# Optimization experiments

Hardware: AMD Instinct MI355X
Metric: run time of the kernel (lower is better)

Reference implementation:

```python
import jax, jax.numpy as jnp
import numpy as np

EPS = 1e-7
BLOCK_SIZE = 128
LN_EPS = 1e-6

def _project(x):
    norm = jnp.maximum(jnp.linalg.norm(x, axis=-1, keepdims=True), EPS)
    max_norm = 1.0 - EPS
    return jnp.where(norm >= 1.0, x / norm * max_norm, x)

def _mobius_add(x, y, c):
    x2 = jnp.sum(x * x, -1, keepdims=True)
    y2 = jnp.sum(y * y, -1, keepdims=True)
    xy = jnp.sum(x * y, -1, keepdims=True)
    num = (1 + 2 * c * xy + c * y2) * x + (1 - c * x2) * y
    den = 1 + 2 * c * xy + c * c * x2 * y2
    return _project(num / jnp.maximum(den, EPS))

def _logmap0(y, c):
    sqrt_c = jnp.maximum(jnp.sqrt(c), EPS)
    y_norm = jnp.linalg.norm(y, axis=-1, keepdims=True)
    safe = jnp.maximum(y_norm, EPS)
    mag = jnp.arctanh(jnp.minimum(y_norm, 1.0 - EPS)) / sqrt_c
    return jnp.where(y_norm < EPS, jnp.zeros_like(y), mag * (y / safe))

def _expmap0(v, c):
    sqrt_c = jnp.maximum(jnp.sqrt(c), EPS)
    v_norm = jnp.linalg.norm(v, axis=-1, keepdims=True)
    safe = jnp.maximum(v_norm, EPS)
    mag = jnp.tanh(sqrt_c * safe) / sqrt_c
    return _project(jnp.where(v_norm < EPS, jnp.zeros_like(v), mag * (v / safe)))

def _dist(x, y, c):
    sqrt_c = jnp.maximum(jnp.sqrt(c), EPS)
    add_norm = jnp.linalg.norm(_mobius_add(-x, y, c), axis=-1)
    sc = jnp.squeeze(sqrt_c, -1)
    arg = jnp.minimum(sc * add_norm, 1.0 - EPS)
    return 2.0 * jnp.arctanh(arg) / sc

def _layernorm(t, scale, bias):
    mu = jnp.mean(t, -1, keepdims=True)
    var = jnp.mean((t - mu) ** 2, -1, keepdims=True)
    return (t - mu) * jax.lax.rsqrt(var + LN_EPS) * scale + bias

def _rope(x, fc):
    # x: [Be, H, bs, hd]; fc: [bs, hd//2] complex
    x_r, x_i = jnp.split(x, 2, -1)
    xc = jax.lax.complex(x_r, x_i)
    rot = xc * fc.reshape(1, 1, fc.shape[0], fc.shape[1])
    return jnp.concatenate([rot.real, rot.imag], -1)

def setup_inputs() -> dict:
    key = jax.random.key(0)
    ks = jax.random.split(key, 8)
    B, N, D, H = 1, 1024, 1024, 16
    w = lambda k, s: jax.random.normal(k, s, jnp.float32) * 0.02
    x = jax.random.normal(ks[0], (B, N, D), jnp.float32) * 0.02  # points inside the ball
    c_global = jax.random.uniform(ks[1], (B, 1), jnp.float32, minval=0.1, maxval=1.0)
    return dict(
        x=x, c_global=c_global,
        qkv_w=w(ks[2], (D, 3 * D)), qkv_b=jnp.zeros((3 * D,), jnp.float32),
        out_w=w(ks[3], (D, D)), out_b=jnp.zeros((D,), jnp.float32),
        ffn_w1=w(ks[4], (D, 4 * D)), ffn_b1=jnp.zeros((4 * D,), jnp.float32),
        ffn_w2=w(ks[5], (4 * D, D)), ffn_b2=jnp.zeros((D,), jnp.float32),
        ln1_scale=jnp.ones((D,), jnp.float32), ln1_bias=jnp.zeros((D,), jnp.float32),
        ln2_scale=jnp.ones((D,), jnp.float32), ln2_bias=jnp.zeros((D,), jnp.float32),
        c_logits=jnp.zeros((H,), jnp.float32),
        geo_scale=jnp.ones((1, H, 1, 1), jnp.float32),
        start_pos=0,
    )

def reference(x, c_global, qkv_w, qkv_b, out_w, out_b, ffn_w1, ffn_b1, ffn_w2, ffn_b2,
              ln1_scale, ln1_bias, ln2_scale, ln2_bias, c_logits, geo_scale, start_pos):
    B, N, D = x.shape
    H = c_logits.shape[0]
    hd = D // H
    bs = BLOCK_SIZE
    nb = N // bs
    Be = B * nb
    xb = x.reshape(Be, bs, D)
    c_b = jnp.repeat(c_global, nb, axis=0).reshape(Be, 1, 1)
    x_res1 = xb
    # tangent-space norm 1 + attention input
    x_norm = _expmap0(_layernorm(_logmap0(xb, c_b), ln1_scale, ln1_bias), c_b)
    x_tan = _logmap0(x_norm, c_b)
    qkv = (x_tan @ qkv_w + qkv_b).reshape(Be, bs, 3, H, hd).transpose(2, 0, 3, 1, 4)
    q, k, v = qkv[0], qkv[1], qkv[2]  # [Be, H, bs, hd]
    # block-local RoPE (module recomputes freqs_cis for h_dim/block_size internally)
    freqs = 1.0 / (10000.0 ** (jnp.arange(0, hd, 2, dtype=jnp.float32) / hd))
    fc = jnp.exp(1j * jnp.outer(jnp.arange(bs), freqs))
    q = _rope(q, fc)
    k = _rope(k, fc)
    c_head = jax.nn.softplus(c_logits).reshape(1, H, 1, 1)
    q_hyp = _expmap0(q, c_head)
    k_hyp = _expmap0(k, c_head)
    d = _dist(q_hyp[:, :, :, None, :], k_hyp[:, :, None, :, :], c_head[:, :, None, :, :])  # [Be,H,bs,bs]
    attn = jax.nn.softmax(-geo_scale * d, axis=-1)
    ao = jnp.einsum('bhqk,bhkd->bhqd', attn, v).transpose(0, 2, 1, 3).reshape(Be, bs, D)
    ao = ao @ out_w + out_b
    x_att = _mobius_add(x_res1, _expmap0(ao, c_b), c_b)
    # tangent-space norm 2 + hyperbolic FFN
    x_norm2 = _expmap0(_layernorm(_logmap0(x_att, c_b), ln2_scale, ln2_bias), c_b)
    t = _logmap0(x_norm2, c_b)
    t = jax.nn.gelu(t @ ffn_w1 + ffn_b1) @ ffn_w2 + ffn_b2
    x_ffn = _expmap0(t, c_b)
    out = _mobius_add(x_att, x_ffn, c_b)
    return out.reshape(B, N, D)
```

## Files before the change

kernel.cpp:

```cpp
#include <hip/hip_runtime.h>

typedef unsigned int uint;
typedef unsigned short ushort;
typedef __attribute__((ext_vector_type(8))) short bf16x8;
typedef __attribute__((ext_vector_type(4))) float f32x4;

#define EPSF 1e-7f
#define ONE_M_EPS 0.99999988079071044921875f
#define ATANH_1ME 8.4056213f
#define Y2_CLIP 0.99999982f

__device__ __forceinline__ ushort f2bf(float f){
  union{float f;uint u;}x; x.f=f; uint u=x.u;
  return (ushort)((u + 0x7fffu + ((u>>16)&1u)) >> 16);
}
__device__ __forceinline__ float bf2f(ushort u){
  union{uint u;float f;}x; x.u = ((uint)u)<<16; return x.f;
}
__device__ __forceinline__ float atanh_c(float a){
  a = fminf(a, ONE_M_EPS);
  return 0.5f*__logf((1.f+a)/(1.f-a));
}
__device__ __forceinline__ float gelu_t(float v){
  return 0.5f*v*(1.f + tanhf(0.7978845608f*(v + 0.044715f*v*v*v)));
}

__device__ __forceinline__ float expmap_factor(float n2, float sc, float& r2){
  float n = sqrtf(n2);
  if (n < EPSF) { r2 = 0.f; return 0.f; }
  float mag = tanhf(sc*n)/sc;
  float f = mag/n;
  if (mag >= 1.f) { f *= ONE_M_EPS/mag; r2 = Y2_CLIP; }
  else r2 = mag*mag;
  return f;
}
__device__ __forceinline__ float roundtrip_factor(float tn2, float sc){
  float tn = sqrtf(tn2);
  if (tn < EPSF) return 0.f;
  float mag = tanhf(sc*tn)/sc;
  if (mag >= 1.f) {
    return ATANH_1ME / (sc * tn);
  } else {
    if (mag < EPSF) return 0.f;
    return (mag/tn) * (atanh_c(mag) / (sc * mag));
  }
}

__device__ __forceinline__ void rope64(float* v, int row){
  #pragma unroll
  for (int i=0;i<32;i++){
    float fr = __expf(-(float)i * 0.28782313662f);
    float sn, cn; __sincosf((float)row * fr, &sn, &cn);
    float a = v[i], b = v[i+32];
    v[i] = a*cn - b*sn;
    v[i+32] = a*sn + b*cn;
  }
}

__device__ __forceinline__ float blkSum(float v, float* tmp){
  #pragma unroll
  for (int o=32;o>0;o>>=1) v += __shfl_xor(v, o, 64);
  int w = threadIdx.x >> 6;
  if ((threadIdx.x & 63) == 0) tmp[w] = v;
  __syncthreads();
  v = tmp[0]+tmp[1]+tmp[2]+tmp[3];
  __syncthreads();
  return v;
}
__device__ __forceinline__ float2 blkSum2(float a, float b, float* tmp){
  #pragma unroll
  for (int o=32;o>0;o>>=1){ a += __shfl_xor(a, o, 64); b += __shfl_xor(b, o, 64); }
  int w = threadIdx.x >> 6;
  if ((threadIdx.x & 63) == 0){ tmp[w] = a; tmp[4+w] = b; }
  __syncthreads();
  float2 r; r.x = tmp[0]+tmp[1]+tmp[2]+tmp[3]; r.y = tmp[4]+tmp[5]+tmp[6]+tmp[7];
  __syncthreads();
  return r;
}

__global__ __launch_bounds__(256) void k_pre(const float* __restrict__ qkv_w,
    const float* __restrict__ out_w, const float* __restrict__ ffn_w1,
    const float* __restrict__ ffn_w2, const float* __restrict__ x,
    const float* __restrict__ cg, const float* __restrict__ lns, const float* __restrict__ lnb,
    ushort* __restrict__ wq, ushort* __restrict__ wo,
    ushort* __restrict__ w1, ushort* __restrict__ w2, ushort* __restrict__ xtan){
  __shared__ float s[32][33];
  int b = blockIdx.x;
  if (b < 12288){
    const float* W; ushort* WT; int K, N;
    if (b < 3072){ W=qkv_w; WT=wq; K=1024; N=3072; }
    else if (b < 4096){ b-=3072; W=out_w; WT=wo; K=1024; N=1024; }
    else if (b < 8192){ b-=4096; W=ffn_w1; WT=w1; K=1024; N=4096; }
    else { b-=8192; W=ffn_w2; WT=w2; K=4096; N=1024; }
    int nbn = N >> 5;
    int n0 = (b % nbn)*32, k0 = (b / nbn)*32;
    int tx = threadIdx.x & 31, ty = threadIdx.x >> 5;
    #pragma unroll
    for (int i=0;i<4;i++)
      s[ty+8*i][tx] = W[(size_t)(k0+ty+8*i)*N + n0+tx];
    __syncthreads();
    #pragma unroll
    for (int i=0;i<4;i++)
      WT[(size_t)(n0+ty+8*i)*K + k0+tx] = f2bf(s[tx][ty+8*i]);
  } else {
    float* tmp = &s[0][0];
    int r = b - 12288, t = threadIdx.x;
    float c = cg[0];
    float sc = fmaxf(sqrtf(c), EPSF);
    float4 xv = ((const float4*)(x + (size_t)r*1024))[t];
    float n2 = blkSum(xv.x*xv.x + xv.y*xv.y + xv.z*xv.z + xv.w*xv.w, tmp);
    float n = sqrtf(n2);
    float f1 = (n < EPSF) ? 0.f : (atanh_c(n) / sc / n);
    float ux = xv.x*f1, uy = xv.y*f1, uz = xv.z*f1, uw = xv.w*f1;
    float2 s12 = blkSum2(ux+uy+uz+uw, ux*ux+uy*uy+uz*uz+uw*uw, tmp);
    float mu = s12.x*(1.f/1024.f);
    float var = s12.y*(1.f/1024.f) - mu*mu;
    float inv = rsqrtf(var + 1e-6f);
    float4 sv = ((const float4*)lns)[t];
    float4 bv = ((const float4*)lnb)[t];
    float ta = (ux-mu)*inv*sv.x + bv.x;
    float tb = (uy-mu)*inv*sv.y + bv.y;
    float tc = (uz-mu)*inv*sv.z + bv.z;
    float td = (uw-mu)*inv*sv.w + bv.w;
    float tn2 = blkSum(ta*ta+tb*tb+tc*tc+td*td, tmp);
    float f = roundtrip_factor(tn2, sc);
    ushort4 o; o.x=f2bf(ta*f); o.y=f2bf(tb*f); o.z=f2bf(tc*f); o.w=f2bf(td*f);
    ((ushort4*)(xtan + (size_t)r*1024))[t] = o;
  }
}

template<int EPI>
__global__ __launch_bounds__(256) void k_gemm(const ushort* __restrict__ A,
    const ushort* __restrict__ Bt, const float* __restrict__ bias,
    void* __restrict__ C, int M, int N, int Kstride, int Kchunk){
  constexpr int MF = 2, NF = 4;
  __shared__ ushort As[2][128*64];
  __shared__ ushort Bs[2][64*64];
  const int tid = threadIdx.x;
  const int lane = tid & 63;
  const int wid = tid >> 6;
  const int ro = wid * 32, co = 0;
  const int l15 = lane & 15, hi = lane >> 4;
  const int nwg = gridDim.x * gridDim.y;
  const int lin = blockIdx.y * gridDim.x + blockIdx.x;
  const int qq = nwg >> 3, rr = nwg & 7;
  const int xcd = lin & 7, ii = lin >> 3;
  const int swz = (xcd < rr) ? (xcd*(qq+1) + ii) : (rr*(qq+1) + (xcd-rr)*qq + ii);
  const int m0 = (swz % gridDim.y) * 128;
  const int n0 = (swz / gridDim.y) * 64;
  const int z = blockIdx.z;
  const int kbase = z * Kchunk;
  const int swr = (l15 & 7) << 3;

  f32x4 acc[MF][NF];
  #pragma unroll
  for (int i=0;i<MF;i++)
    #pragma unroll
    for (int j=0;j<NF;j++) acc[i][j] = (f32x4){0.f,0.f,0.f,0.f};

  auto stage = [&](int buf, int koff){
    #pragma unroll
    for (int r2=0;r2<4;r2++){
      int idx = r2*256 + tid;
      int row = idx >> 3, cc = idx & 7;
      int off = koff + ((cc ^ (row & 7)) << 3);
      const ushort* ga = A + (size_t)(m0+row)*Kstride + off;
      int lo = (r2*256 + (tid & 192)) * 8;
      __builtin_amdgcn_global_load_lds((const __attribute__((address_space(1))) uint*)ga,
          (__attribute__((address_space(3))) uint*)&As[buf][lo], 16, 0, 0);
    }
    #pragma unroll
    for (int r2=0;r2<2;r2++){
      int idx = r2*256 + tid;
      int row = idx >> 3, cc = idx & 7;
      int off = koff + ((cc ^ (row & 7)) << 3);
      const ushort* gb = Bt + (size_t)(n0+row)*Kstride + off;
      int lo = (r2*256 + (tid & 192)) * 8;
      __builtin_amdgcn_global_load_lds((const __attribute__((address_space(1))) uint*)gb,
          (__attribute__((address_space(3))) uint*)&Bs[buf][lo], 16, 0, 0);
    }
  };
  auto compute = [&](int buf){
    #pragma unroll
    for (int ks=0;ks<2;ks++){
      bf16x8 af[MF], bfv[NF];
      int cb = (ks*32 + hi*8) ^ swr;
      #pragma unroll
      for (int m2=0;m2<MF;m2++) af[m2]  = *(const bf16x8*)&As[buf][(ro+m2*16+l15)*64 + cb];
      #pragma unroll
      for (int n2=0;n2<NF;n2++) bfv[n2] = *(const bf16x8*)&Bs[buf][(co+n2*16+l15)*64 + cb];
      #pragma unroll
      for (int m2=0;m2<MF;m2++)
        #pragma unroll
        for (int n2=0;n2<NF;n2++)
          acc[m2][n2] = __builtin_amdgcn_mfma_f32_16x16x32_bf16(af[m2], bfv[n2], acc[m2][n2], 0, 0, 0);
    }
  };

  const int nt = Kchunk >> 6;
  stage(0, kbase);
  __syncthreads();
  int cur = 0;
  for (int t = 1; t < nt; ++t){
    stage(cur ^ 1, kbase + t*64);
    compute(cur);
    __syncthreads();
    cur ^= 1;
  }
  compute(cur);

  #pragma unroll
  for (int m=0;m<MF;m++){
    #pragma unroll
    for (int n=0;n<NF;n++){
      int gc = n0 + co + n*16 + l15;
      float bb = (EPI == 3) ? (z == 0 ? bias[gc] : 0.f) : bias[gc];
      #pragma unroll
      for (int i=0;i<4;i++){
        int gr = m0 + ro + m*16 + hi*4 + i;
        float v = acc[m][n][i] + bb;
        if (EPI == 2) v = gelu_t(v);
        if (EPI == 2) ((ushort*)C)[(size_t)gr*N + gc] = f2bf(v);
        else ((float*)C)[(size_t)z*M*N + (size_t)gr*N + gc] = v;
      }
    }
  }
}

__global__ __launch_bounds__(128) void k_attn4(const float* __restrict__ qkv,
    const float* __restrict__ c_logits, const float* __restrict__ geo,
    ushort* __restrict__ ao){
  constexpr size_t PSTRIDE = (size_t)1024*3072;
  __shared__ ushort Kh[128*64], Kl[128*64];
  __shared__ ushort Vth[64*128], Vtl[64*128];
  __shared__ ushort Qh[32*64], Ql[32*64];
  __shared__ float k2s[128], q2s[32];
  const int h = blockIdx.x, be = blockIdx.y, qs = blockIdx.z;
  const int tid = threadIdx.x;
  const float cl = c_logits[h];
  const float ch = (cl > 20.f) ? cl : log1pf(__expf(cl));
  const float sc = fmaxf(sqrtf(ch), EPSF);
  const float gs = geo[h];

  {
    int kv = tid;
    const float4* pa = (const float4*)(qkv + (size_t)(be*128+kv)*3072 + 1024 + h*64);
    const float4* pb = (const float4*)(qkv + PSTRIDE + (size_t)(be*128+kv)*3072 + 1024 + h*64);
    float v[64];
    #pragma unroll
    for (int c=0;c<16;c++){
      float4 ta = pa[c], tb = pb[c];
      v[4*c]=ta.x+tb.x; v[4*c+1]=ta.y+tb.y; v[4*c+2]=ta.z+tb.z; v[4*c+3]=ta.w+tb.w;
    }
    rope64(v, kv);
    float n2 = 0.f;
    #pragma unroll
    for (int e=0;e<64;e++) n2 += v[e]*v[e];
    float r2; float f = expmap_factor(n2, sc, r2);
    k2s[kv] = r2;
    #pragma unroll
    for (int cch=0; cch<8; cch++){
      uint4 uh, ul;
      uint hw[4], lw[4];
      #pragma unroll
      for (int w2=0; w2<4; w2++){
        float a0 = v[cch*8 + w2*2] * f, a1 = v[cch*8 + w2*2 + 1] * f;
        ushort h0 = f2bf(a0); ushort l0 = f2bf(a0 - bf2f(h0));
        ushort h1 = f2bf(a1); ushort l1 = f2bf(a1 - bf2f(h1));
        hw[w2] = (uint)h0 | ((uint)h1<<16);
        lw[w2] = (uint)l0 | ((uint)l1<<16);
      }
      uh.x=hw[0]; uh.y=hw[1]; uh.z=hw[2]; uh.w=hw[3];
      ul.x=lw[0]; ul.y=lw[1]; ul.z=lw[2]; ul.w=lw[3];
      int idx = kv*64 + ((cch ^ (kv&7))<<3);
      *(uint4*)&Kh[idx] = uh;
      *(uint4*)&Kl[idx] = ul;
    }
  }
  {
    int kv = tid;
    const float4* pa = (const float4*)(qkv + (size_t)(be*128+kv)*3072 + 2048 + h*64);
    const float4* pb = (const float4*)(qkv + PSTRIDE + (size_t)(be*128+kv)*3072 + 2048 + h*64);
    float v[64];
    #pragma unroll
    for (int c=0;c<16;c++){
      float4 ta = pa[c], tb = pb[c];
      v[4*c]=ta.x+tb.x; v[4*c+1]=ta.y+tb.y; v[4*c+2]=ta.z+tb.z; v[4*c+3]=ta.w+tb.w;
    }
    #pragma unroll
    for (int d=0; d<64; d++){
      float a = v[d];
      ushort hh = f2bf(a); ushort ll = f2bf(a - bf2f(hh));
      int idx = d*128 + (((kv>>3) ^ (d&7))<<3) + (kv&7);
      Vth[idx] = hh; Vtl[idx] = ll;
    }
  }
  if (tid < 32){
    int qrow = qs*32 + tid;
    const float4* pa = (const float4*)(qkv + (size_t)(be*128+qrow)*3072 + h*64);
    const float4* pb = (const float4*)(qkv + PSTRIDE + (size_t)(be*128+qrow)*3072 + h*64);
    float v[64];
    #pragma unroll
    for (int c=0;c<16;c++){
      float4 ta = pa[c], tb = pb[c];
      v[4*c]=ta.x+tb.x; v[4*c+1]=ta.y+tb.y; v[4*c+2]=ta.z+tb.z; v[4*c+3]=ta.w+tb.w;
    }
    rope64(v, qrow);
    float n2 = 0.f;
    #pragma unroll
    for (int e=0;e<64;e++) n2 += v[e]*v[e];
    float r2; float f = expmap_factor(n2, sc, r2);
    q2s[tid] = r2;
    #pragma unroll
    for (int cch=0; cch<8; cch++){
      uint4 uh, ul;
      uint hw[4], lw[4];
      #pragma unroll
      for (int w2=0; w2<4; w2++){
        float a0 = v[cch*8 + w2*2] * f, a1 = v[cch*8 + w2*2 + 1] * f;
        ushort h0 = f2bf(a0); ushort l0 = f2bf(a0 - bf2f(h0));
        ushort h1 = f2bf(a1); ushort l1 = f2bf(a1 - bf2f(h1));
        hw[w2] = (uint)h0 | ((uint)h1<<16);
        lw[w2] = (uint)l0 | ((uint)l1<<16);
      }
      uh.x=hw[0]; uh.y=hw[1]; uh.z=hw[2]; uh.w=hw[3];
      ul.x=lw[0]; ul.y=lw[1]; ul.z=lw[2]; ul.w=lw[3];
      int idx = tid*64 + ((cch ^ (tid&7))<<3);
      *(uint4*)&Qh[idx] = uh;
      *(uint4*)&Ql[idx] = ul;
    }
  }
  __syncthreads();

  const int lane = tid & 63, w = tid >> 6;
  const int l15 = lane & 15, hi4 = lane >> 4;
  f32x4 acc[8];
  #pragma unroll
  for (int nf=0;nf<8;nf++) acc[nf] = (f32x4){0.f,0.f,0.f,0.f};
  #pragma unroll
  for (int ks=0; ks<2; ks++){
    int qrowL = w*16 + l15;
    int qidx = qrowL*64 + (((ks*4 + hi4) ^ (qrowL&7))<<3);
    bf16x8 qh = *(const bf16x8*)&Qh[qidx];
    bf16x8 ql2 = *(const bf16x8*)&Ql[qidx];
    #pragma unroll
    for (int nf=0; nf<8; nf++){
      int krow = nf*16 + l15;
      int kidx = krow*64 + (((ks*4 + hi4) ^ (krow&7))<<3);
      bf16x8 kh = *(const bf16x8*)&Kh[kidx];
      bf16x8 kl2 = *(const bf16x8*)&Kl[kidx];
      acc[nf] = __builtin_amdgcn_mfma_f32_16x16x32_bf16(qh, kh, acc[nf], 0, 0, 0);
      acc[nf] = __builtin_amdgcn_mfma_f32_16x16x32_bf16(qh, kl2, acc[nf], 0, 0, 0);
      acc[nf] = __builtin_amdgcn_mfma_f32_16x16x32_bf16(ql2, kh, acc[nf], 0, 0, 0);
    }
  }
  __syncthreads();

  float q2v[4], Bfv[4];
  #pragma unroll
  for (int i=0;i<4;i++){ q2v[i] = q2s[w*16 + hi4*4 + i]; Bfv[i] = 1.f - ch*q2v[i]; }
  const float e2 = 2.f*ch;
  #pragma unroll
  for (int nf=0; nf<8; nf++){
    float k2 = k2s[nf*16 + l15];
    #pragma unroll
    for (int i=0;i<4;i++){
      float xy = acc[nf][i];
      float Af = 1.f + ch*k2 - e2*xy;
      float den = fmaxf(Af - ch*k2*Bfv[i], EPSF);
      float num2 = fmaxf(Af*(Af*q2v[i] - 2.f*Bfv[i]*xy) + Bfv[i]*Bfv[i]*k2, 0.f);
      float rn = sqrtf(num2)/den;
      rn = (rn >= 1.f) ? ONE_M_EPS : rn;
      float arg = fminf(sc*rn, ONE_M_EPS);
      float dd = __logf((1.f+arg)/(1.f-arg)) / sc;
      acc[nf][i] = -gs*dd;
    }
  }
  #pragma unroll
  for (int i=0;i<4;i++){
    float m = acc[0][i];
    #pragma unroll
    for (int nf=1;nf<8;nf++) m = fmaxf(m, acc[nf][i]);
    #pragma unroll
    for (int o=1;o<16;o<<=1) m = fmaxf(m, __shfl_xor(m, o));
    float l = 0.f;
    #pragma unroll
    for (int nf=0;nf<8;nf++){ float pp = __expf(acc[nf][i]-m); acc[nf][i] = pp; l += pp; }
    #pragma unroll
    for (int o=1;o<16;o<<=1) l += __shfl_xor(l, o);
    float inv = 1.f/l;
    #pragma unroll
    for (int nf=0;nf<8;nf++){
      float p = acc[nf][i]*inv;
      ushort ph = f2bf(p);
      ushort pl = f2bf(p - bf2f(ph));
      int row = w*16 + hi4*4 + i, col = nf*16 + l15;
      int idx = row*128 + (((col>>3) ^ (row&7))<<3) + (col&7);
      Kh[idx] = ph; Kl[idx] = pl;
    }
  }
  __syncthreads();

  f32x4 acc2[4];
  #pragma unroll
  for (int nf=0;nf<4;nf++) acc2[nf] = (f32x4){0.f,0.f,0.f,0.f};
  #pragma unroll
  for (int ks=0; ks<4; ks++){
    int prow = w*16 + l15;
    int pidx = prow*128 + (((ks*4 + hi4) ^ (prow&7))<<3);
    bf16x8 ph = *(const bf16x8*)&Kh[pidx];
    bf16x8 pl = *(const bf16x8*)&Kl[pidx];
    #pragma unroll
    for (int nf=0; nf<4; nf++){
      int vrow = nf*16 + l15;
      int vidx = vrow*128 + (((ks*4 + hi4) ^ (vrow&7))<<3);
      bf16x8 vh = *(const bf16x8*)&Vth[vidx];
      bf16x8 vl = *(const bf16x8*)&Vtl[vidx];
      acc2[nf] = __builtin_amdgcn_mfma_f32_16x16x32_bf16(ph, vh, acc2[nf], 0, 0, 0);
      acc2[nf] = __builtin_amdgcn_mfma_f32_16x16x32_bf16(ph, vl, acc2[nf], 0, 0, 0);
      acc2[nf] = __builtin_amdgcn_mfma_f32_16x16x32_bf16(pl, vh, acc2[nf], 0, 0, 0);
    }
  }
  #pragma unroll
  for (int nf=0; nf<4; nf++)
    #pragma unroll
    for (int i=0;i<4;i++){
      int row = qs*32 + w*16 + hi4*4 + i;
      int col = nf*16 + l15;
      ao[(size_t)(be*128 + row)*1024 + h*64 + col] = f2bf(acc2[nf][i]);
    }
}

__global__ __launch_bounds__(256) void k_postattn(const float* __restrict__ x,
    const float* __restrict__ proj, const float* __restrict__ cg,
    const float* __restrict__ lns, const float* __restrict__ lnb,
    float* __restrict__ xatt, ushort* __restrict__ tout){
  __shared__ float tmp[8];
  int r = blockIdx.x, t = threadIdx.x;
  float c = cg[0], sc = fmaxf(sqrtf(c), EPSF);
  float4 pa = ((const float4*)(proj + (size_t)r*1024))[t];
  float4 pb = ((const float4*)(proj + 1024*1024 + (size_t)r*1024))[t];
  float4 pc = ((const float4*)(proj + 2*1024*1024 + (size_t)r*1024))[t];
  float4 pd = ((const float4*)(proj + 3*1024*1024 + (size_t)r*1024))[t];
  float4 pv; pv.x=(pa.x+pb.x)+(pc.x+pd.x); pv.y=(pa.y+pb.y)+(pc.y+pd.y);
  pv.z=(pa.z+pb.z)+(pc.z+pd.z); pv.w=(pa.w+pb.w)+(pc.w+pd.w);
  float4 xv = ((const float4*)(x + (size_t)r*1024))[t];
  float pn2 = blkSum(pv.x*pv.x+pv.y*pv.y+pv.z*pv.z+pv.w*pv.w, tmp);
  float y2; float fy = expmap_factor(pn2, sc, y2);
  float ya = pv.x*fy, yb = pv.y*fy, yc = pv.z*fy, yd = pv.w*fy;
  float2 s = blkSum2(xv.x*xv.x+xv.y*xv.y+xv.z*xv.z+xv.w*xv.w,
                     xv.x*ya+xv.y*yb+xv.z*yc+xv.w*yd, tmp);
  float x2 = s.x, xy = s.y;
  float Af = 1.f + 2.f*c*xy + c*y2;
  float Bf = 1.f - c*x2;
  float den = fmaxf(1.f + 2.f*c*xy + c*c*x2*y2, EPSF);
  float num2 = fmaxf(Af*Af*x2 + 2.f*Af*Bf*xy + Bf*Bf*y2, 0.f);
  float rn = sqrtf(num2)/den;
  float fp = (rn >= 1.f) ? (ONE_M_EPS/fmaxf(rn,EPSF)) : 1.f;
  float xan = (rn >= 1.f) ? ONE_M_EPS : rn;
  float g = fp/den;
  float xa = (Af*xv.x + Bf*ya)*g;
  float xb = (Af*xv.y + Bf*yb)*g;
  float xc = (Af*xv.z + Bf*yc)*g;
  float xd = (Af*xv.w + Bf*yd)*g;
  float4 xo; xo.x=xa; xo.y=xb; xo.z=xc; xo.w=xd;
  ((float4*)(xatt + (size_t)r*1024))[t] = xo;
  float at = (rn >= 1.f) ? ATANH_1ME : atanh_c(xan);
  float fl = (xan < EPSF) ? 0.f : at / sc / fmaxf(xan, EPSF);
  float ux = xa*fl, uy = xb*fl, uz = xc*fl, uw = xd*fl;
  float2 s12 = blkSum2(ux+uy+uz+uw, ux*ux+uy*uy+uz*uz+uw*uw, tmp);
  float mu = s12.x*(1.f/1024.f);
  float var = s12.y*(1.f/1024.f) - mu*mu;
  float inv = rsqrtf(var + 1e-6f);
  float4 sv = ((const float4*)lns)[t];
  float4 bv = ((const float4*)lnb)[t];
  float ta = (ux-mu)*inv*sv.x + bv.x;
  float tb = (uy-mu)*inv*sv.y + bv.y;
  float tc = (uz-mu)*inv*sv.z + bv.z;
  float td = (uw-mu)*inv*sv.w + bv.w;
  float tn2 = blkSum(ta*ta+tb*tb+tc*tc+td*td, tmp);
  float f = roundtrip_factor(tn2, sc);
  ushort4 o; o.x=f2bf(ta*f); o.y=f2bf(tb*f); o.z=f2bf(tc*f); o.w=f2bf(td*f);
  ((ushort4*)(tout + (size_t)r*1024))[t] = o;
}

__global__ __launch_bounds__(256) void k_final(const float* __restrict__ xatt,
    const float* __restrict__ tf, const float* __restrict__ cg, float* __restrict__ out){
  __shared__ float tmp[8];
  int r = blockIdx.x, t = threadIdx.x;
  float c = cg[0], sc = fmaxf(sqrtf(c), EPSF);
  float4 fa = ((const float4*)(tf + (size_t)r*1024))[t];
  float4 fb = ((const float4*)(tf + 1024*1024 + (size_t)r*1024))[t];
  float4 fc = ((const float4*)(tf + 2*1024*1024 + (size_t)r*1024))[t];
  float4 fd = ((const float4*)(tf + 3*1024*1024 + (size_t)r*1024))[t];
  float4 fv; fv.x=(fa.x+fb.x)+(fc.x+fd.x); fv.y=(fa.y+fb.y)+(fc.y+fd.y);
  fv.z=(fa.z+fb.z)+(fc.z+fd.z); fv.w=(fa.w+fb.w)+(fc.w+fd.w);
  float4 xv = ((const float4*)(xatt + (size_t)r*1024))[t];
  float fn2 = blkSum(fv.x*fv.x+fv.y*fv.y+fv.z*fv.z+fv.w*fv.w, tmp);
  float y2; float fy = expmap_factor(fn2, sc, y2);
  float ya = fv.x*fy, yb = fv.y*fy, yc = fv.z*fy, yd = fv.w*fy;
  float2 s = blkSum2(xv.x*xv.x+xv.y*xv.y+xv.z*xv.z+xv.w*xv.w,
                     xv.x*ya+xv.y*yb+xv.z*yc+xv.w*yd, tmp);
  float x2 = s.x, xy = s.y;
  float Af = 1.f + 2.f*c*xy + c*y2;
  float Bf = 1.f - c*x2;
  float den = fmaxf(1.f + 2.f*c*xy + c*c*x2*y2, EPSF);
  float num2 = fmaxf(Af*Af*x2 + 2.f*Af*Bf*xy + Bf*Bf*y2, 0.f);
  float rn = sqrtf(num2)/den;
  float fp = (rn >= 1.f) ? (ONE_M_EPS/fmaxf(rn,EPSF)) : 1.f;
  float g = fp/den;
  float4 o;
  o.x = (Af*xv.x + Bf*ya)*g;
  o.y = (Af*xv.y + Bf*yb)*g;
  o.z = (Af*xv.z + Bf*yc)*g;
  o.w = (Af*xv.w + Bf*yd)*g;
  ((float4*)(out + (size_t)r*1024))[t] = o;
}

extern "C" void kernel_launch(void* const* d_in, const int* in_sizes, int n_in,
                              void* d_out, int out_size, void* d_ws, size_t ws_size,
                              hipStream_t stream){
  (void)in_sizes; (void)n_in; (void)out_size; (void)ws_size;
  const float* x     = (const float*)d_in[0];
  const float* cg    = (const float*)d_in[1];
  const float* qkv_w = (const float*)d_in[2];
  const float* qkv_b = (const float*)d_in[3];
  const float* out_w = (const float*)d_in[4];
  const float* out_b = (const float*)d_in[5];
  const float* ffn_w1= (const float*)d_in[6];
  const float* ffn_b1= (const float*)d_in[7];
  const float* ffn_w2= (const float*)d_in[8];
  const float* ffn_b2= (const float*)d_in[9];
  const float* ln1s  = (const float*)d_in[10];
  const float* ln1b  = (const float*)d_in[11];
  const float* ln2s  = (const float*)d_in[12];
  const float* ln2b  = (const float*)d_in[13];
  const float* clog  = (const float*)d_in[14];
  const float* geo   = (const float*)d_in[15];

  char* p = (char*)d_ws;
  auto take = [&](size_t n){ char* r = p; p += (n + 255) & ~(size_t)255; return r; };
  ushort* wt_qkv  = (ushort*)take((size_t)3072*1024*2);
  ushort* wt_out  = (ushort*)take((size_t)1024*1024*2);
  ushort* wt_ffn1 = (ushort*)take((size_t)4096*1024*2);
  ushort* wt_ffn2 = (ushort*)take((size_t)1024*4096*2);
  float*  bufA    = (float*)take((size_t)2*1024*3072*4);
  ushort* bufB    = (ushort*)take((size_t)1024*1024*2);
  float*  bufC    = (float*)take((size_t)4*1024*1024*4);
  float*  xatt    = (float*)take((size_t)1024*1024*4);
  ushort* tbuf    = (ushort*)take((size_t)1024*1024*2);

  k_pre<<<13312, 256, 0, stream>>>(qkv_w, out_w, ffn_w1, ffn_w2, x, cg, ln1s, ln1b,
                                   wt_qkv, wt_out, wt_ffn1, wt_ffn2, bufB);
  k_gemm<3><<<dim3(48,8,2), 256, 0, stream>>>(bufB, wt_qkv, qkv_b, (void*)bufA, 1024, 3072, 1024, 512);
  k_attn4<<<dim3(16,8,4), 128, 0, stream>>>(bufA, clog, geo, bufB);
  k_gemm<3><<<dim3(16,8,4), 256, 0, stream>>>(bufB, wt_out, out_b, (void*)bufC, 1024, 1024, 1024, 256);
  k_postattn<<<1024, 256, 0, stream>>>(x, bufC, cg, ln2s, ln2b, xatt, tbuf);
  k_gemm<2><<<dim3(64,8,1), 256, 0, stream>>>(tbuf, wt_ffn1, ffn_b1, (void*)bufA, 1024, 4096, 1024, 1024);
  k_gemm<3><<<dim3(16,8,4), 256, 0, stream>>>((const ushort*)bufA, wt_ffn2, ffn_b2, (void*)bufC, 1024, 1024, 4096, 1024);
  k_final<<<1024, 256, 0, stream>>>(xatt, bufC, cg, (float*)d_out);
}
```

Measured before the change: 123.4 us.

## Process 64 queries per attention block with role-split warps and single-bf16 V

The attention kernel now runs 256 threads over 64 query rows per block instead of 128 threads over 32. This halves the number of blocks that redundantly rebuild K and V shared tiles per head. Thread groups are split by role: one group builds K, one transposes V, one builds Q, so these prologue stages run concurrently. V is stored only as a high bf16 part, which drops one MFMA per step and some shared memory at a small precision cost, and RoPE frequencies come from a constant table instead of per-element exp.

```diff
diff --git a/kernel.cpp b/kernel.cpp
--- a/kernel.cpp
+++ b/kernel.cpp
@@ -46,11 +46,21 @@
   }
 }
 
+__device__ __constant__ float FREQS[32] = {
+  1.0f, 0.7498942093324559f, 0.5623413251903491f, 0.4216965034285822f,
+  0.31622776601683794f, 0.23713737056616552f, 0.1778279410038923f, 0.13335214321633242f,
+  0.1f, 0.07498942093324558f, 0.05623413251903491f, 0.04216965034285822f,
+  0.03162277660168379f, 0.023713737056616554f, 0.01778279410038923f, 0.013335214321633242f,
+  0.01f, 0.007498942093324559f, 0.005623413251903491f, 0.004216965034285822f,
+  0.0031622776601683794f, 0.0023713737056616554f, 0.0017782794100389228f, 0.0013335214321633241f,
+  0.001f, 0.0007498942093324558f, 0.0005623413251903491f, 0.0004216965034285822f,
+  0.00031622776601683794f, 0.00023713737056616553f, 0.00017782794100389227f, 0.00013335214321633243f
+};
+
 __device__ __forceinline__ void rope64(float* v, int row){
   #pragma unroll
   for (int i=0;i<32;i++){
-    float fr = __expf(-(float)i * 0.28782313662f);
-    float sn, cn; __sincosf((float)row * fr, &sn, &cn);
+    float sn, cn; __sincosf((float)row * FREQS[i], &sn, &cn);
     float a = v[i], b = v[i+32];
     v[i] = a*cn - b*sn;
     v[i+32] = a*sn + b*cn;
@@ -227,14 +237,14 @@
   }
 }
 
-__global__ __launch_bounds__(128) void k_attn4(const float* __restrict__ qkv,
+__global__ __launch_bounds__(256) void k_attn5(const float* __restrict__ qkv,
     const float* __restrict__ c_logits, const float* __restrict__ geo,
     ushort* __restrict__ ao){
   constexpr size_t PSTRIDE = (size_t)1024*3072;
   __shared__ ushort Kh[128*64], Kl[128*64];
-  __shared__ ushort Vth[64*128], Vtl[64*128];
-  __shared__ ushort Qh[32*64], Ql[32*64];
-  __shared__ float k2s[128], q2s[32];
+  __shared__ ushort Vth[64*128];
+  __shared__ ushort Qh[64*64], Ql[64*64];
+  __shared__ float k2s[128], q2s[64];
   const int h = blockIdx.x, be = blockIdx.y, qs = blockIdx.z;
   const int tid = threadIdx.x;
   const float cl = c_logits[h];
@@ -242,7 +252,7 @@
   const float sc = fmaxf(sqrtf(ch), EPSF);
   const float gs = geo[h];
 
-  {
+  if (tid < 128){
     int kv = tid;
     const float4* pa = (const float4*)(qkv + (size_t)(be*128+kv)*3072 + 1024 + h*64);
     const float4* pb = (const float4*)(qkv + PSTRIDE + (size_t)(be*128+kv)*3072 + 1024 + h*64);
@@ -260,7 +270,6 @@
     k2s[kv] = r2;
     #pragma unroll
     for (int cch=0; cch<8; cch++){
-      uint4 uh, ul;
       uint hw[4], lw[4];
       #pragma unroll
       for (int w2=0; w2<4; w2++){
@@ -270,50 +279,49 @@
         hw[w2] = (uint)h0 | ((uint)h1<<16);
         lw[w2] = (uint)l0 | ((uint)l1<<16);
       }
-      uh.x=hw[0]; uh.y=hw[1]; uh.z=hw[2]; uh.w=hw[3];
-      ul.x=lw[0]; ul.y=lw[1]; ul.z=lw[2]; ul.w=lw[3];
+      uint4 uh; uh.x=hw[0]; uh.y=hw[1]; uh.z=hw[2]; uh.w=hw[3];
+      uint4 ul; ul.x=lw[0]; ul.y=lw[1]; ul.z=lw[2]; ul.w=lw[3];
       int idx = kv*64 + ((cch ^ (kv&7))<<3);
       *(uint4*)&Kh[idx] = uh;
       *(uint4*)&Kl[idx] = ul;
     }
-  }
-  {
-    int kv = tid;
-    const float4* pa = (const float4*)(qkv + (size_t)(be*128+kv)*3072 + 2048 + h*64);
-    const float4* pb = (const float4*)(qkv + PSTRIDE + (size_t)(be*128+kv)*3072 + 2048 + h*64);
+  } else if (tid < 192){
+    #pragma unroll
+    for (int rr2=0; rr2<2; rr2++){
+      int kv = (tid - 128) + rr2*64;
+      const float4* pa = (const float4*)(qkv + (size_t)(be*128+kv)*3072 + 2048 + h*64);
+      const float4* pb = (const float4*)(qkv + PSTRIDE + (size_t)(be*128+kv)*3072 + 2048 + h*64);
+      float v[64];
+      #pragma unroll
+      for (int c=0;c<16;c++){
+        float4 ta = pa[c], tb = pb[c];
+        v[4*c]=ta.x+tb.x; v[4*c+1]=ta.y+tb.y; v[4*c+2]=ta.z+tb.z; v[4*c+3]=ta.w+tb.w;
+      }
+      #pragma unroll
+      for (int d=0; d<64; d++){
+        int idx = d*128 + (((kv>>3) ^ (d&7))<<3) + (kv&7);
+        Vth[idx] = f2bf(v[d]);
+      }
+    }
+  } else {
+    int ql = tid - 192;
+    int qrow = qs*64 + ql;
+    const float4* pa = (const float4*)(qkv + (size_t)(be*128+qrow)*3072 + h*64);
+    const float4* pb = (const float4*)(qkv + PSTRIDE + (size_t)(be*128+qrow)*3072 + h*64);
     float v[64];
     #pragma unroll
     for (int c=0;c<16;c++){
       float4 ta = pa[c], tb = pb[c];
       v[4*c]=ta.x+tb.x; v[4*c+1]=ta.y+tb.y; v[4*c+2]=ta.z+tb.z; v[4*c+3]=ta.w+tb.w;
     }
-    #pragma unroll
-    for (int d=0; d<64; d++){
-      float a = v[d];
-      ushort hh = f2bf(a); ushort ll = f2bf(a - bf2f(hh));
-      int idx = d*128 + (((kv>>3) ^ (d&7))<<3) + (kv&7);
-      Vth[idx] = hh; Vtl[idx] = ll;
-    }
-  }
-  if (tid < 32){
-    int qrow = qs*32 + tid;
-    const float4* pa = (const float4*)(qkv + (size_t)(be*128+qrow)*3072 + h*64);
-    const float4* pb = (const float4*)(qkv + PSTRIDE + (size_t)(be*128+qrow)*3072 + h*64);
-    float v[64];
-    #pragma unroll
-    for (int c=0;c<16;c++){
-      float4 ta = pa[c], tb = pb[c];
-      v[4*c]=ta.x+tb.x; v[4*c+1]=ta.y+tb.y; v[4*c+2]=ta.z+tb.z; v[4*c+3]=ta.w+tb.w;
-    }
     rope64(v, qrow);
     float n2 = 0.f;
     #pragma unroll
     for (int e=0;e<64;e++) n2 += v[e]*v[e];
     float r2; float f = expmap_factor(n2, sc, r2);
-    q2s[tid] = r2;
+    q2s[ql] = r2;
     #pragma unroll
     for (int cch=0; cch<8; cch++){
-      uint4 uh, ul;
       uint hw[4], lw[4];
       #pragma unroll
       for (int w2=0; w2<4; w2++){
@@ -323,9 +331,9 @@
         hw[w2] = (uint)h0 | ((uint)h1<<16);
         lw[w2] = (uint)l0 | ((uint)l1<<16);
       }
-      uh.x=hw[0]; uh.y=hw[1]; uh.z=hw[2]; uh.w=hw[3];
-      ul.x=lw[0]; ul.y=lw[1]; ul.z=lw[2]; ul.w=lw[3];
-      int idx = tid*64 + ((cch ^ (tid&7))<<3);
+      uint4 uh; uh.x=hw[0]; uh.y=hw[1]; uh.z=hw[2]; uh.w=hw[3];
+      uint4 ul; ul.x=lw[0]; ul.y=lw[1]; ul.z=lw[2]; ul.w=lw[3];
+      int idx = ql*64 + ((cch ^ (ql&7))<<3);
       *(uint4*)&Qh[idx] = uh;
       *(uint4*)&Ql[idx] = ul;
     }
@@ -415,9 +423,7 @@
       int vrow = nf*16 + l15;
       int vidx = vrow*128 + (((ks*4 + hi4) ^ (vrow&7))<<3);
       bf16x8 vh = *(const bf16x8*)&Vth[vidx];
-      bf16x8 vl = *(const bf16x8*)&Vtl[vidx];
       acc2[nf] = __builtin_amdgcn_mfma_f32_16x16x32_bf16(ph, vh, acc2[nf], 0, 0, 0);
-      acc2[nf] = __builtin_amdgcn_mfma_f32_16x16x32_bf16(ph, vl, acc2[nf], 0, 0, 0);
       acc2[nf] = __builtin_amdgcn_mfma_f32_16x16x32_bf16(pl, vh, acc2[nf], 0, 0, 0);
     }
   }
@@ -425,7 +431,7 @@
   for (int nf=0; nf<4; nf++)
     #pragma unroll
     for (int i=0;i<4;i++){
-      int row = qs*32 + w*16 + hi4*4 + i;
+      int row = qs*64 + w*16 + hi4*4 + i;
       int col = nf*16 + l15;
       ao[(size_t)(be*128 + row)*1024 + h*64 + col] = f2bf(acc2[nf][i]);
     }
@@ -553,7 +559,7 @@
   k_pre<<<13312, 256, 0, stream>>>(qkv_w, out_w, ffn_w1, ffn_w2, x, cg, ln1s, ln1b,
                                    wt_qkv, wt_out, wt_ffn1, wt_ffn2, bufB);
   k_gemm<3><<<dim3(48,8,2), 256, 0, stream>>>(bufB, wt_qkv, qkv_b, (void*)bufA, 1024, 3072, 1024, 512);
-  k_attn4<<<dim3(16,8,4), 128, 0, stream>>>(bufA, clog, geo, bufB);
+  k_attn5<<<dim3(16,8,2), 256, 0, stream>>>(bufA, clog, geo, bufB);
   k_gemm<3><<<dim3(16,8,4), 256, 0, stream>>>(bufB, wt_out, out_b, (void*)bufC, 1024, 1024, 1024, 256);
   k_postattn<<<1024, 256, 0, stream>>>(x, bufC, cg, ln2s, ln2b, xatt, tbuf);
   k_gemm<2><<<dim3(64,8,1), 256, 0, stream>>>(tbuf, wt_ffn1, ffn_b1, (void*)bufA, 1024, 4096, 1024, 1024);
```

Measured after the change: 116.6 us. 5.5% less time.
